# Kernel optimization log

Hardware: AMD Instinct MI355X
Metric: run time of the kernel (lower is better)

Reference implementation:

```python
import jax, jax.numpy as jnp
import numpy as np

B, T, D, K = 8, 2048, 256, 8192
COMMITMENT_COST = 0.25

def setup_inputs() -> dict:
    key = jax.random.key(0)
    k1, k2 = jax.random.split(key)
    xs = jax.random.normal(k1, (B, T, D), dtype=jnp.float32)
    # lengths: all full so max(ilens) == T and the wrapper slice is a no-op (static shapes for jit)
    ilens = jnp.full((B,), T, dtype=jnp.int64)
    codebook = jax.random.normal(k2, (K, D), dtype=jnp.float32)
    return {"xs": xs, "ilens": ilens, "codebook": codebook}

def reference(xs, ilens, codebook):
    # Quantizer.forward: slice xs to max(ilens) (no-op here, max(ilens)==T),
    # then VectorQuantize: euclidean nearest-codebook search + commitment loss.
    x_sq = jnp.sum(xs * xs, axis=-1, keepdims=True)              # (B, T, 1)
    c_sq = jnp.sum(codebook * codebook, axis=-1)                 # (K,)
    dots = jnp.einsum('btd,kd->btk', xs, codebook)               # (B, T, K)
    dist = x_sq - 2.0 * dots + c_sq                              # (B, T, K)
    indices = jnp.argmin(dist, axis=-1)                          # (B, T)
    quantized = codebook[indices]                                # (B, T, D) gather
    # commitment loss: mse(quantize.detach(), x)
    diff = jax.lax.stop_gradient(quantized) - xs
    commit_loss = jnp.mean(diff * diff)
    loss = COMMITMENT_COST * commit_loss
    return (loss, commit_loss)
```

## Files before the change

### kernel.cpp

```cpp
#include <hip/hip_runtime.h>
#include <stdint.h>

#define M_TOK 16384
#define DIM   256
#define KCB   8192
#define NGRP  8
#define GRP   1024
#define NCHK  16
#define NT    16
#define SHIFT 512.0f
#define INV_N (1.0f / 4194304.0f)
#define SC1   0x7F7F7F7F

typedef __attribute__((ext_vector_type(4))) float f32x4;
typedef __attribute__((ext_vector_type(8))) int   i32x8;

static __device__ __forceinline__ void lds_cp16(const void* g, void* l) {
    __builtin_amdgcn_global_load_lds(
        (const __attribute__((address_space(1))) void*)g,
        (__attribute__((address_space(3))) void*)l, 16, 0, 0);
}

static __device__ __forceinline__ int pk4(float4 f) {
    int o = __builtin_amdgcn_cvt_pk_fp8_f32(f.x, f.y, 0, false);
    o     = __builtin_amdgcn_cvt_pk_fp8_f32(f.z, f.w, o, true);
    return o;
}

__global__ void k_prep(const float* __restrict__ cb,
                       unsigned char* __restrict__ cbt,
                       float* __restrict__ chalf) {
    __shared__ float part[4][64];
    const int w  = threadIdx.x >> 6;
    const int l  = threadIdx.x & 63;
    const int c0 = blockIdx.x * 64;
    const float* row = cb + (size_t)(c0 + l) * DIM;
    float s = 0.0f;
    #pragma unroll
    for (int j = 0; j < 4; j++) {
        int ch = w * 4 + j;
        const float* p = row + ch * 16;
        float4 a = *(const float4*)(p);
        float4 b = *(const float4*)(p + 4);
        float4 c = *(const float4*)(p + 8);
        float4 d = *(const float4*)(p + 12);
        s += a.x*a.x + a.y*a.y + a.z*a.z + a.w*a.w
           + b.x*b.x + b.y*b.y + b.z*b.z + b.w*b.w
           + c.x*c.x + c.y*c.y + c.z*c.z + c.w*c.w
           + d.x*d.x + d.y*d.y + d.z*d.z + d.w*d.w;
        float4 na = {-a.x, -a.y, -a.z, -a.w};
        float4 nb = {-b.x, -b.y, -b.z, -b.w};
        float4 nc = {-c.x, -c.y, -c.z, -c.w};
        float4 nd = {-d.x, -d.y, -d.z, -d.w};
        uint4 r;
        r.x = (unsigned)pk4(na); r.y = (unsigned)pk4(nb);
        r.z = (unsigned)pk4(nc); r.w = (unsigned)pk4(nd);
        *(uint4*)(cbt + ((size_t)ch * KCB + c0 + l) * 16) = r;
    }
    part[w][l] = s;
    __syncthreads();
    if (w == 0) {
        float t = part[0][l] + part[1][l] + part[2][l] + part[3][l];
        chalf[c0 + l] = 0.5f * t + SHIFT;
    }
}

__global__ __launch_bounds__(256, 4) void k_gemm_argmin(
    const float* __restrict__ xs,
    const unsigned char* __restrict__ cbt,
    const float* __restrict__ chalf,
    uint32_t* __restrict__ pkey)
{
    __shared__ __align__(16) unsigned char Bs[2][NCHK][64][16];
    __shared__ float schalf[GRP];

    const int tid  = threadIdx.x;
    const int w    = tid >> 6;
    const int l    = tid & 63;
    const int lrow = l & 15;
    const int quad = l >> 4;
    const int m0 = blockIdx.x * 128;
    const int g  = blockIdx.y;

    *(float4*)&schalf[tid * 4] = ((const float4*)(chalf + g * GRP))[tid];

    const unsigned char* bsrc = cbt + ((size_t)(w * 4) * KCB + g * GRP + l) * 16;

    #pragma unroll
    for (int j = 0; j < 4; j++)
        lds_cp16(bsrc + (size_t)j * KCB * 16, &Bs[0][w * 4 + j][0][0]);

    i32x8 afr[2][2];
    {
        const float* ap = xs + (size_t)(m0 + w * 32 + lrow) * DIM + quad * 32;
        #pragma unroll
        for (int rt = 0; rt < 2; rt++)
            #pragma unroll
            for (int ks = 0; ks < 2; ks++) {
                const float* p = ap + rt * 16 * DIM + ks * 128;
                union { int d[8]; i32x8 v; } aa;
                #pragma unroll
                for (int d = 0; d < 8; d++)
                    aa.d[d] = pk4(*(const float4*)(p + d * 4));
                afr[rt][ks] = aa.v;
            }
    }

    uint32_t best[2][4];
    #pragma unroll
    for (int rt = 0; rt < 2; rt++)
        #pragma unroll
        for (int rg = 0; rg < 4; rg++) best[rt][rg] = 0xFFFFFFFFu;

    #pragma unroll 1
    for (int t = 0; t < NT; t++) {
        const int cur = t & 1;
        __syncthreads();
        if (t < NT - 1) {
            #pragma unroll
            for (int j = 0; j < 4; j++)
                lds_cp16(bsrc + ((size_t)j * KCB + (t + 1) * 64) * 16,
                         &Bs[1 - cur][w * 4 + j][0][0]);
        }

        f32x4 acc[2][4];
        #pragma unroll
        for (int ct = 0; ct < 4; ct++) {
            float cs = schalf[t * 64 + ct * 16 + lrow];
            #pragma unroll
            for (int rt = 0; rt < 2; rt++) {
                f32x4 c4 = {cs, cs, cs, cs};
                acc[rt][ct] = c4;
            }
        }
        #pragma unroll
        for (int ks = 0; ks < 2; ks++) {
            const int ch = ks * 8 + quad * 2;
            i32x8 bfr[4];
            #pragma unroll
            for (int ct = 0; ct < 4; ct++) {
                union { uint4 q[2]; i32x8 v; } bb;
                bb.q[0] = *(const uint4*)&Bs[cur][ch][ct * 16 + lrow][0];
                bb.q[1] = *(const uint4*)&Bs[cur][ch + 1][ct * 16 + lrow][0];
                bfr[ct] = bb.v;
            }
            #pragma unroll
            for (int rt = 0; rt < 2; rt++)
                #pragma unroll
                for (int ct = 0; ct < 4; ct++)
                    acc[rt][ct] = __builtin_amdgcn_mfma_scale_f32_16x16x128_f8f6f4(
                        afr[rt][ks], bfr[ct], acc[rt][ct],
                        0, 0,
                        0, SC1,
                        0, SC1);
        }
        #pragma unroll
        for (int ct = 0; ct < 4; ct++) {
            uint32_t idl = (uint32_t)(t * 64 + ct * 16 + lrow);
            #pragma unroll
            for (int rt = 0; rt < 2; rt++)
                #pragma unroll
                for (int rg = 0; rg < 4; rg++) {
                    uint32_t key =
                        (__float_as_uint(acc[rt][ct][rg]) & 0xFFFFFC00u) | idl;
                    if (key < best[rt][rg]) best[rt][rg] = key;
                }
        }
    }

    #pragma unroll
    for (int off = 1; off < 16; off <<= 1)
        #pragma unroll
        for (int rt = 0; rt < 2; rt++)
            #pragma unroll
            for (int rg = 0; rg < 4; rg++) {
                uint32_t o = __shfl_xor(best[rt][rg], off);
                if (o < best[rt][rg]) best[rt][rg] = o;
            }
    if (lrow == 0) {
        #pragma unroll
        for (int rt = 0; rt < 2; rt++)
            #pragma unroll
            for (int rg = 0; rg < 4; rg++)
                pkey[(size_t)(m0 + w * 32 + rt * 16 + quad * 4 + rg) * NGRP + g]
                    = best[rt][rg];
    }
}

__global__ void k_finalize(const uint32_t* __restrict__ pkey,
                           const float4* __restrict__ xs4,
                           const float4* __restrict__ cb4,
                           float* __restrict__ partial) {
    __shared__ float sblk[4];
    int w   = threadIdx.x >> 6;
    int row = blockIdx.x * 4 + w;
    int l   = threadIdx.x & 63;
    uint32_t k = 0xFFFFFFFFu;
    int g = 0;
    if (l < 8) { k = pkey[(size_t)row * NGRP + l]; g = l; }
    #pragma unroll
    for (int off = 1; off < 8; off <<= 1) {
        uint32_t ok = __shfl_xor(k, off);
        int      og = __shfl_xor(g, off);
        if (ok < k) { k = ok; g = og; }
    }
    k = __shfl(k, 0);
    g = __shfl(g, 0);
    int code = g * GRP + (int)(k & 1023u);
    float4 x = xs4[(size_t)row * 64 + l];
    float4 c = cb4[(size_t)code * 64 + l];
    float dx = x.x - c.x, dy = x.y - c.y, dz = x.z - c.z, dw = x.w - c.w;
    float s = dx * dx + dy * dy + dz * dz + dw * dw;
    #pragma unroll
    for (int off = 32; off; off >>= 1) s += __shfl_xor(s, off);
    if (l == 0) sblk[w] = s;
    __syncthreads();
    if (threadIdx.x == 0)
        partial[blockIdx.x] = sblk[0] + sblk[1] + sblk[2] + sblk[3];
}

__global__ void k_write(const float* __restrict__ partial,
                        float* __restrict__ out) {
    __shared__ float swv[16];
    int tid = threadIdx.x;
    float s = partial[tid] + partial[tid + 1024] +
              partial[tid + 2048] + partial[tid + 3072];
    #pragma unroll
    for (int off = 32; off; off >>= 1) s += __shfl_xor(s, off);
    if ((tid & 63) == 0) swv[tid >> 6] = s;
    __syncthreads();
    if (tid == 0) {
        float t = 0.0f;
        #pragma unroll
        for (int i = 0; i < 16; i++) t += swv[i];
        float commit = t * INV_N;
        out[0] = 0.25f * commit;
        out[1] = commit;
    }
}

extern "C" void kernel_launch(void* const* d_in, const int* in_sizes, int n_in,
                              void* d_out, int out_size, void* d_ws, size_t ws_size,
                              hipStream_t stream) {
    const float* xs = (const float*)d_in[0];
    const float* cb = (const float*)d_in[2];

    char* ws = (char*)d_ws;
    unsigned char* cbt     = (unsigned char*)(ws + 256);
    float*         chalf   = (float*)(ws + 256 + 2097152);
    uint32_t*      pkey    = (uint32_t*)(ws + 256 + 2129920);
    float*         partial = (float*)(ws + 256 + 2654208);

    k_prep<<<128, 256, 0, stream>>>(cb, cbt, chalf);
    dim3 g(M_TOK / 128, NGRP);
    k_gemm_argmin<<<g, 256, 0, stream>>>(xs, cbt, chalf, pkey);
    k_finalize<<<4096, 256, 0, stream>>>(pkey, (const float4*)xs,
                                         (const float4*)cb, partial);
    k_write<<<1, 1024, 0, stream>>>(partial, (float*)d_out);
}
```

Baseline: 119.5 us.

## Load codebook fragments directly from global into registers, drop LDS staging

Removes the double-buffered LDS staging of the fp8 codebook tile, which used global_load_lds plus a per-iteration barrier. Each lane now reads its B fragments straight from global/L2 into registers and feeds them to the MFMAs, with the loop unrolled by two to help hide latency. This removes barriers and LDS traffic but makes every wave redundantly fetch the same codebook bytes from cache. Register pressure rises, so launch bounds drop from 4 to 3 waves per SIMD.

```diff
diff --git a/kernel.cpp b/kernel.cpp
--- a/kernel.cpp
+++ b/kernel.cpp
@@ -14,12 +14,6 @@
 
 typedef __attribute__((ext_vector_type(4))) float f32x4;
 typedef __attribute__((ext_vector_type(8))) int   i32x8;
-
-static __device__ __forceinline__ void lds_cp16(const void* g, void* l) {
-    __builtin_amdgcn_global_load_lds(
-        (const __attribute__((address_space(1))) void*)g,
-        (__attribute__((address_space(3))) void*)l, 16, 0, 0);
-}
 
 static __device__ __forceinline__ int pk4(float4 f) {
     int o = __builtin_amdgcn_cvt_pk_fp8_f32(f.x, f.y, 0, false);
@@ -65,13 +59,12 @@
     }
 }
 
-__global__ __launch_bounds__(256, 4) void k_gemm_argmin(
+__global__ __launch_bounds__(256, 3) void k_gemm_argmin(
     const float* __restrict__ xs,
     const unsigned char* __restrict__ cbt,
     const float* __restrict__ chalf,
     uint32_t* __restrict__ pkey)
 {
-    __shared__ __align__(16) unsigned char Bs[2][NCHK][64][16];
     __shared__ float schalf[GRP];
 
     const int tid  = threadIdx.x;
@@ -84,11 +77,8 @@
 
     *(float4*)&schalf[tid * 4] = ((const float4*)(chalf + g * GRP))[tid];
 
-    const unsigned char* bsrc = cbt + ((size_t)(w * 4) * KCB + g * GRP + l) * 16;
-
-    #pragma unroll
-    for (int j = 0; j < 4; j++)
-        lds_cp16(bsrc + (size_t)j * KCB * 16, &Bs[0][w * 4 + j][0][0]);
+    const unsigned char* bbase =
+        cbt + ((size_t)(quad * 2) * KCB + g * GRP + lrow) * 16;
 
     i32x8 afr[2][2];
     {
@@ -112,16 +102,21 @@
         #pragma unroll
         for (int rg = 0; rg < 4; rg++) best[rt][rg] = 0xFFFFFFFFu;
 
-    #pragma unroll 1
+    __syncthreads();
+
+    #pragma unroll 2
     for (int t = 0; t < NT; t++) {
-        const int cur = t & 1;
-        __syncthreads();
-        if (t < NT - 1) {
-            #pragma unroll
-            for (int j = 0; j < 4; j++)
-                lds_cp16(bsrc + ((size_t)j * KCB + (t + 1) * 64) * 16,
-                         &Bs[1 - cur][w * 4 + j][0][0]);
-        }
+        const unsigned char* bt = bbase + (size_t)t * 64 * 16;
+
+        uint4 braw[2][4][2];
+        #pragma unroll
+        for (int ks = 0; ks < 2; ks++)
+            #pragma unroll
+            for (int ct = 0; ct < 4; ct++)
+                #pragma unroll
+                for (int h = 0; h < 2; h++)
+                    braw[ks][ct][h] = *(const uint4*)(
+                        bt + ((size_t)(ks * 8 + h) * KCB + ct * 16) * 16);
 
         f32x4 acc[2][4];
         #pragma unroll
@@ -134,26 +129,20 @@
             }
         }
         #pragma unroll
-        for (int ks = 0; ks < 2; ks++) {
-            const int ch = ks * 8 + quad * 2;
-            i32x8 bfr[4];
+        for (int ks = 0; ks < 2; ks++)
             #pragma unroll
             for (int ct = 0; ct < 4; ct++) {
                 union { uint4 q[2]; i32x8 v; } bb;
-                bb.q[0] = *(const uint4*)&Bs[cur][ch][ct * 16 + lrow][0];
-                bb.q[1] = *(const uint4*)&Bs[cur][ch + 1][ct * 16 + lrow][0];
-                bfr[ct] = bb.v;
-            }
-            #pragma unroll
-            for (int rt = 0; rt < 2; rt++)
-                #pragma unroll
-                for (int ct = 0; ct < 4; ct++)
+                bb.q[0] = braw[ks][ct][0];
+                bb.q[1] = braw[ks][ct][1];
+                #pragma unroll
+                for (int rt = 0; rt < 2; rt++)
                     acc[rt][ct] = __builtin_amdgcn_mfma_scale_f32_16x16x128_f8f6f4(
-                        afr[rt][ks], bfr[ct], acc[rt][ct],
+                        afr[rt][ks], bb.v, acc[rt][ct],
                         0, 0,
                         0, SC1,
                         0, SC1);
-        }
+            }
         #pragma unroll
         for (int ct = 0; ct < 4; ct++) {
             uint32_t idl = (uint32_t)(t * 64 + ct * 16 + lrow);
```

Measured after the change: 150.0 us. 1.25x slower.
